# Kernel optimization log

Hardware: AMD Instinct MI355X
Metric: run time of the kernel (lower is better)

Reference implementation:

```python
import jax, jax.numpy as jnp
import numpy as np

B, N, EPG, FDIM, H = 128, 512, 4096, 128, 128
RATIO = 0.5
E = B * EPG
K1 = int(np.ceil(RATIO * N))      # 256
K2 = int(np.ceil(RATIO * K1))     # 128
K3 = int(np.ceil(RATIO * K2))     # 64


def setup_inputs():
    key = jax.random.key(0)
    ks = jax.random.split(key, 12)
    x = jax.random.normal(ks[0], (B * N, FDIM), jnp.float32)
    src = jax.random.randint(ks[1], (B, EPG), 0, N)
    dst = jax.random.randint(ks[2], (B, EPG), 0, N)
    off = (jnp.arange(B) * N)[:, None]
    edge_index = jnp.stack([(src + off).reshape(-1), (dst + off).reshape(-1)], 0).astype(jnp.int32)
    batch = (jnp.arange(B * N) // N).astype(jnp.int32)
    w = lambda k, s: jax.random.normal(k, s, jnp.float32) * 0.05
    return dict(
        x=x, edge_index=edge_index, batch=batch,
        W1=w(ks[3], (FDIM, H)), b1=jnp.zeros((H,), jnp.float32),
        Ws1=w(ks[4], (H, 1)), bs1=jnp.zeros((1,), jnp.float32),
        W2=w(ks[5], (H, H)), b2=jnp.zeros((H,), jnp.float32),
        Ws2=w(ks[6], (H, 1)), bs2=jnp.zeros((1,), jnp.float32),
        W3=w(ks[7], (H, H)), b3=jnp.zeros((H,), jnp.float32),
        Ws3=w(ks[8], (H, 1)), bs3=jnp.zeros((1,), jnp.float32))


def gcn(x, src, dst, emask, W, b):
    # PyG GCNConv: add self-loops, symmetric deg^-1/2 normalization.
    n = x.shape[0]
    h = x @ W
    deg = jnp.zeros((n,), x.dtype).at[dst].add(emask) + 1.0  # +1 for self-loop
    dinv = jax.lax.rsqrt(deg)
    norm = dinv[src] * dinv[dst] * emask                      # masked edges -> 0
    agg = jnp.zeros_like(h).at[dst].add(norm[:, None] * h[src])
    return agg + (dinv * dinv)[:, None] * h + b               # self-loop term + bias


def sag_pool(x, src, dst, emask, Ws, bs, n_per_graph, k):
    n_tot = x.shape[0]
    score = gcn(x, src, dst, emask, Ws, bs)[:, 0]
    sc = score.reshape(B, n_per_graph)
    topv, topi = jax.lax.top_k(sc, k)                         # [B,k] per-graph topk
    xg = x.reshape(B, n_per_graph, -1)
    xnew = jnp.take_along_axis(xg, topi[:, :, None], axis=1) * jnp.tanh(topv)[:, :, None]
    xnew = xnew.reshape(B * k, -1)
    perm = (topi + (jnp.arange(B) * n_per_graph)[:, None]).reshape(-1)
    newidx = jnp.full((n_tot,), -1, jnp.int32).at[perm].set(jnp.arange(B * k, dtype=jnp.int32))
    ns, nd = newidx[src], newidx[dst]
    valid = (ns >= 0) & (nd >= 0)
    emask_new = emask * valid.astype(x.dtype)                 # filter_adj via masking
    ns = jnp.where(valid, ns, 0)
    nd = jnp.where(valid, nd, 0)
    return xnew, ns, nd, emask_new


def readout(x, k):
    xg = x.reshape(B, k, -1)
    return jnp.concatenate([xg.max(axis=1), xg.mean(axis=1)], axis=1)  # [gmp, gap]


def reference(x, edge_index, batch, W1, b1, Ws1, bs1, W2, b2, Ws2, bs2, W3, b3, Ws3, bs3):
    src, dst = edge_index[0], edge_index[1]
    emask = jnp.ones((src.shape[0],), x.dtype)
    h = jax.nn.relu(gcn(x, src, dst, emask, W1, b1))
    h, src, dst, emask = sag_pool(h, src, dst, emask, Ws1, bs1, N, K1)
    x1 = readout(h, K1)
    h = jax.nn.relu(gcn(h, src, dst, emask, W2, b2))
    h, src, dst, emask = sag_pool(h, src, dst, emask, Ws2, bs2, K1, K2)
    x2 = readout(h, K2)
    h = jax.nn.relu(gcn(h, src, dst, emask, W3, b3))
    h, src, dst, emask = sag_pool(h, src, dst, emask, Ws3, bs3, K2, K3)
    x3 = readout(h, K3)
    return x1 + x2 + x3
```

## Files before the change

kernel.cpp:

```cpp
#include <hip/hip_runtime.h>
#include <math.h>

#define BGRAPH 128
#define ETOT   (128*4096)
#define EPG    4096
#define K1 256
#define K2 128
#define K3 64

__global__ __launch_bounds__(256) void gemm_tile3(const float* __restrict__ X,
                                                  const float* __restrict__ W,
                                                  float* __restrict__ Y){
  __shared__ float sA[128][33];
  __shared__ float sB[32][192];
  int t = threadIdx.x;
  int row0 = blockIdx.x * 128;
  int tx = t & 15;
  int ty = t >> 4;
  float acc[8][8];
  #pragma unroll
  for (int i = 0; i < 8; ++i)
    #pragma unroll
    for (int j = 0; j < 8; ++j) acc[i][j] = 0.f;

  for (int k0 = 0; k0 < 128; k0 += 32){
    #pragma unroll
    for (int i = 0; i < 4; ++i){
      int f = t + i*256;
      int row = f >> 3, c4 = f & 7;
      float4 v = *(const float4*)(X + (size_t)(row0 + row)*128 + k0 + c4*4);
      sA[row][c4*4+0] = v.x;
      sA[row][c4*4+1] = v.y;
      sA[row][c4*4+2] = v.z;
      sA[row][c4*4+3] = v.w;
    }
    #pragma unroll
    for (int i = 0; i < 4; ++i){
      int f = t + i*256;
      int kr = f >> 5, c4 = f & 31;
      int gg = c4 >> 1, hh = c4 & 1;
      float4 v = *(const float4*)(W + (size_t)(k0 + kr)*128 + c4*4);
      *(float4*)&sB[kr][gg*12 + hh*4] = v;
    }
    __syncthreads();
    #pragma unroll
    for (int kk = 0; kk < 32; ++kk){
      float4 b0 = *(const float4*)&sB[kk][tx*12];
      float4 b1 = *(const float4*)&sB[kk][tx*12 + 4];
      float aa[8];
      #pragma unroll
      for (int i = 0; i < 8; ++i) aa[i] = sA[ty*8 + i][kk];
      float bb[8] = {b0.x,b0.y,b0.z,b0.w,b1.x,b1.y,b1.z,b1.w};
      #pragma unroll
      for (int i = 0; i < 8; ++i)
        #pragma unroll
        for (int j = 0; j < 8; ++j)
          acc[i][j] = fmaf(aa[i], bb[j], acc[i][j]);
    }
    __syncthreads();
  }
  #pragma unroll
  for (int i = 0; i < 8; ++i){
    float* yr = Y + (size_t)(row0 + ty*8 + i)*128 + tx*8;
    *(float4*)yr       = *(float4*)&acc[i][0];
    *(float4*)(yr + 4) = *(float4*)&acc[i][4];
  }
}

__global__ __launch_bounds__(256) void fused_l1(const float* __restrict__ X,
    const float* __restrict__ W, float* __restrict__ Y,
    const int* __restrict__ src, const int* __restrict__ dst,
    int* __restrict__ off, int* __restrict__ cnt, float* __restrict__ dinv,
    int* __restrict__ csr, int* __restrict__ dsto, float* __restrict__ coef,
    int* __restrict__ ecnt){
  extern __shared__ float smem[];
  int t = threadIdx.x;
  if (blockIdx.x < 512){
    float* sA = smem;
    float* sB = smem + 128*33;
    int row0 = blockIdx.x * 128;
    int tx = t & 15;
    int ty = t >> 4;
    float acc[8][8];
    #pragma unroll
    for (int i = 0; i < 8; ++i)
      #pragma unroll
      for (int j = 0; j < 8; ++j) acc[i][j] = 0.f;

    for (int k0 = 0; k0 < 128; k0 += 32){
      #pragma unroll
      for (int i = 0; i < 4; ++i){
        int f = t + i*256;
        int row = f >> 3, c4 = f & 7;
        float4 v = *(const float4*)(X + (size_t)(row0 + row)*128 + k0 + c4*4);
        sA[row*33 + c4*4+0] = v.x;
        sA[row*33 + c4*4+1] = v.y;
        sA[row*33 + c4*4+2] = v.z;
        sA[row*33 + c4*4+3] = v.w;
      }
      #pragma unroll
      for (int i = 0; i < 4; ++i){
        int f = t + i*256;
        int kr = f >> 5, c4 = f & 31;
        int gg = c4 >> 1, hh = c4 & 1;
        float4 v = *(const float4*)(W + (size_t)(k0 + kr)*128 + c4*4);
        *(float4*)&sB[kr*192 + gg*12 + hh*4] = v;
      }
      __syncthreads();
      #pragma unroll
      for (int kk = 0; kk < 32; ++kk){
        float4 b0 = *(const float4*)&sB[kk*192 + tx*12];
        float4 b1 = *(const float4*)&sB[kk*192 + tx*12 + 4];
        float aa[8];
        #pragma unroll
        for (int i = 0; i < 8; ++i) aa[i] = sA[(ty*8 + i)*33 + kk];
        float bb[8] = {b0.x,b0.y,b0.z,b0.w,b1.x,b1.y,b1.z,b1.w};
        #pragma unroll
        for (int i = 0; i < 8; ++i)
          #pragma unroll
          for (int j = 0; j < 8; ++j)
            acc[i][j] = fmaf(aa[i], bb[j], acc[i][j]);
      }
      __syncthreads();
    }
    #pragma unroll
    for (int i = 0; i < 8; ++i){
      float* yr = Y + (size_t)(row0 + ty*8 + i)*128 + tx*8;
      *(float4*)yr       = *(float4*)&acc[i][0];
      *(float4*)(yr + 4) = *(float4*)&acc[i][4];
    }
  } else {
    int g = blockIdx.x - 512;
    int*   sc  = (int*)smem;
    int*   sp  = sc + 512;
    int*   cur = sp + 256;
    float* sdv = (float*)(cur + 512);
    int*   ss  = (int*)(sdv + 512);
    int*   sd  = ss + 4096;
    sc[t] = 0; sc[t + 256] = 0;
    __syncthreads();
    const int* sg = src + g*EPG;
    const int* dg = dst + g*EPG;
    for (int e = t; e < EPG; e += 256){
      int s = sg[e], d = dg[e];
      ss[e] = s; sd[e] = d;
      atomicAdd(&sc[d & 511], 1);
    }
    __syncthreads();
    int a = sc[2*t], b = sc[2*t+1];
    int pair = a + b;
    sp[t] = pair;
    __syncthreads();
    for (int d = 1; d < 256; d <<= 1){
      int u = (t >= d) ? sp[t-d] : 0;
      __syncthreads();
      sp[t] += u;
      __syncthreads();
    }
    int pre0 = sp[t] - pair;
    int pre1 = pre0 + a;
    float dv0 = rsqrtf((float)a + 1.f);
    float dv1 = rsqrtf((float)b + 1.f);
    sdv[2*t]   = dv0;  sdv[2*t+1] = dv1;
    dinv[g*512 + 2*t]   = dv0;  dinv[g*512 + 2*t+1] = dv1;
    cnt[g*512 + 2*t]    = a;    cnt[g*512 + 2*t+1]  = b;
    off[g*512 + 2*t]    = g*EPG + pre0;
    off[g*512 + 2*t+1]  = g*EPG + pre1;
    sc[2*t] = pre0; sc[2*t+1] = pre1;
    cur[2*t] = 0;   cur[2*t+1] = 0;
    if (t == 0) ecnt[g] = EPG;
    __syncthreads();
    int* cg = csr + g*EPG;
    int* dg2 = dsto + g*EPG;
    float* cf = coef + g*EPG;
    for (int e = t; e < EPG; e += 256){
      int s = ss[e], dl = sd[e] & 511;
      int slot = sc[dl] + atomicAdd(&cur[dl], 1);
      cg[slot]  = s;
      dg2[slot] = g*512 + dl;
      cf[slot]  = sdv[s & 511] * sdv[dl];
    }
  }
}

__global__ void gather_agg(const float* __restrict__ hx, const int* __restrict__ csr,
                           const float* __restrict__ coef,
                           const int* __restrict__ off, const int* __restrict__ cnt,
                           const float* __restrict__ dinv, const float* __restrict__ bias,
                           const float* __restrict__ Ws, float* __restrict__ out,
                           float* __restrict__ hs, int npg, int n){
  int bpg = npg >> 3;
  int x = blockIdx.x >> 3, r = blockIdx.x & 7;
  int pos = x % bpg, grp = x / bpg;
  int g = grp*8 + r;
  int t = threadIdx.x;
  int node = g*npg + pos*8 + (t >> 5);
  int fl = t & 31;
  float dd = dinv[node];
  int o = off[node], deg = cnt[node];
  const float4* rows = (const float4*)hx;
  float4 a0 = {0,0,0,0}, a1 = {0,0,0,0}, a2 = {0,0,0,0}, a3 = {0,0,0,0};
  int e = o, end = o + deg;
  for (; e + 7 < end; e += 8){
    int sx[8]; float cx[8]; float4 vv[8];
    #pragma unroll
    for (int q = 0; q < 8; ++q){ sx[q] = csr[e+q]; cx[q] = coef[e+q]; }
    #pragma unroll
    for (int q = 0; q < 8; ++q) vv[q] = rows[(size_t)sx[q]*32 + fl];
    #pragma unroll
    for (int q = 0; q < 8; ++q){
      float4& aq = (q&3)==0 ? a0 : ((q&3)==1 ? a1 : ((q&3)==2 ? a2 : a3));
      aq.x = fmaf(cx[q], vv[q].x, aq.x);
      aq.y = fmaf(cx[q], vv[q].y, aq.y);
      aq.z = fmaf(cx[q], vv[q].z, aq.z);
      aq.w = fmaf(cx[q], vv[q].w, aq.w);
    }
  }
  for (; e + 3 < end; e += 4){
    int sx[4]; float cx[4]; float4 vv[4];
    #pragma unroll
    for (int q = 0; q < 4; ++q){ sx[q] = csr[e+q]; cx[q] = coef[e+q]; }
    #pragma unroll
    for (int q = 0; q < 4; ++q) vv[q] = rows[(size_t)sx[q]*32 + fl];
    #pragma unroll
    for (int q = 0; q < 4; ++q){
      float4& aq = (q==0) ? a0 : ((q==1) ? a1 : ((q==2) ? a2 : a3));
      aq.x = fmaf(cx[q], vv[q].x, aq.x);
      aq.y = fmaf(cx[q], vv[q].y, aq.y);
      aq.z = fmaf(cx[q], vv[q].z, aq.z);
      aq.w = fmaf(cx[q], vv[q].w, aq.w);
    }
  }
  for (; e < end; ++e){
    int s0 = csr[e];
    float c0 = coef[e];
    float4 v0 = rows[(size_t)s0*32 + fl];
    a0.x=fmaf(c0,v0.x,a0.x); a0.y=fmaf(c0,v0.y,a0.y); a0.z=fmaf(c0,v0.z,a0.z); a0.w=fmaf(c0,v0.w,a0.w);
  }
  float4 own = rows[(size_t)node*32 + fl];
  float4 bv  = ((const float4*)bias)[fl];
  float d2 = dd*dd;
  float4 rr;
  rr.x = fmaxf(fmaf(d2, own.x, (a0.x+a1.x)+(a2.x+a3.x) + bv.x), 0.f);
  rr.y = fmaxf(fmaf(d2, own.y, (a0.y+a1.y)+(a2.y+a3.y) + bv.y), 0.f);
  rr.z = fmaxf(fmaf(d2, own.z, (a0.z+a1.z)+(a2.z+a3.z) + bv.z), 0.f);
  rr.w = fmaxf(fmaf(d2, own.w, (a0.w+a1.w)+(a2.w+a3.w) + bv.w), 0.f);
  ((float4*)(out + (size_t)node*128))[fl] = rr;
  float4 w = ((const float4*)Ws)[fl];
  float p = rr.x*w.x + rr.y*w.y + rr.z*w.z + rr.w*w.w;
  p += __shfl_xor(p, 16);
  p += __shfl_xor(p, 8);
  p += __shfl_xor(p, 4);
  p += __shfl_xor(p, 2);
  p += __shfl_xor(p, 1);
  if (fl == 0) hs[node] = p;
}

template<int NP, int K, int HASNEXT, int FIRST>
__global__ __launch_bounds__(1024) void mega(
    const float* __restrict__ hs, const int* __restrict__ csr_in,
    const int* __restrict__ dst_in, const float* __restrict__ coef_in,
    const int* __restrict__ off_in, const int* __restrict__ cnt_in,
    const float* __restrict__ dinv_in, const float* __restrict__ bs,
    const float* __restrict__ Hm, float* __restrict__ xnew, float* __restrict__ out,
    const int* __restrict__ ecnt_in,
    int* __restrict__ off_o, int* __restrict__ cnt_o, float* __restrict__ dinv_o,
    int* __restrict__ csr_o, int* __restrict__ dst_o, float* __restrict__ coef_o,
    int* __restrict__ ecnt_o)
{
  constexpr int R   = 1024 / NP;
  constexpr int LNP = (NP == 512) ? 9 : ((NP == 256) ? 8 : 7);
  __shared__ int   ss[EPG];
  __shared__ int   sd[EPG];
  __shared__ float scf[EPG];
  __shared__ float shs[NP];
  __shared__ float spart[1024];
  __shared__ float sv[NP];
  __shared__ int   si[NP];
  __shared__ int   lnew[NP];
  __shared__ int   lperm[K];
  __shared__ float ltanh[K];
  __shared__ float smx[1024], ssm[1024];
  __shared__ int   sc[K], sp2[K], cur[K];
  __shared__ float sdvn[K];
  int g = blockIdx.x, t = threadIdx.x;
  int E_in = ecnt_in[g];

  if (t < NP){ shs[t] = hs[g*NP + t]; lnew[t] = -1; }
  for (int e = t; e < E_in; e += 1024){
    ss[e]  = csr_in[g*EPG + e];
    sd[e]  = dst_in[g*EPG + e];
    scf[e] = coef_in[g*EPG + e];
  }
  __syncthreads();

  int n = t & (NP-1);
  int p = t >> LNP;
  {
    int lo = off_in[g*NP + n] - g*EPG, deg = cnt_in[g*NP + n];
    float a = 0.f;
    for (int e = lo + p; e < lo + deg; e += R)
      a = fmaf(scf[e], shs[ss[e] & (NP-1)], a);
    spart[t] = a;
  }
  __syncthreads();
  float v = -INFINITY; int idx = n;
  if (p == 0){
    float a = spart[n];
    #pragma unroll
    for (int q = 1; q < R; ++q) a += spart[n + q*NP];
    float dd = dinv_in[g*NP + n];
    v = a + fmaf(dd*dd, shs[n], bs[0]);
  }
  #pragma unroll
  for (int ksz = 2; ksz <= NP; ksz <<= 1){
    #pragma unroll
    for (int j = ksz >> 1; j > 0; j >>= 1){
      float v2 = 0.f; int i2 = 0;
      if (j >= 64){
        __syncthreads();
        if (t < NP){ sv[t] = v; si[t] = idx; }
        __syncthreads();
        if (t < NP){ v2 = sv[t^j]; i2 = si[t^j]; }
      } else if (t < NP){
        v2 = __shfl_xor(v, j);
        i2 = __shfl_xor(idx, j);
      }
      if (t < NP){
        bool dir = ((t & ksz) == 0);
        bool pf = (v2 > v) || (v2 == v && i2 < idx);
        bool lower = (t & j) == 0;
        if (pf == (lower ? dir : !dir)){ v = v2; idx = i2; }
      }
    }
  }
  if (t < K){
    lperm[t] = idx;
    lnew[idx] = t;
    ltanh[t] = tanhf(v);
  }
  __syncthreads();

  {
    int f = t & 127, q = t >> 7;
    float mx = -INFINITY, sm = 0.f;
    for (int j = q; j < K; j += 8){
      float val = Hm[(size_t)(g*NP + lperm[j])*128 + f] * ltanh[j];
      xnew[(size_t)(g*K + j)*128 + f] = val;
      mx = fmaxf(mx, val); sm += val;
    }
    smx[t] = mx; ssm[t] = sm;
  }
  __syncthreads();
  if (t < 128){
    float mx = smx[t], sm = ssm[t];
    #pragma unroll
    for (int q = 1; q < 8; ++q){ mx = fmaxf(mx, smx[q*128+t]); sm += ssm[q*128+t]; }
    if (FIRST){
      out[g*256 + t]       = mx;
      out[g*256 + 128 + t] = sm / (float)K;
    } else {
      out[g*256 + t]       += mx;
      out[g*256 + 128 + t] += sm / (float)K;
    }
  }
  if (!HASNEXT) return;
  __syncthreads();

  if (t < K) sc[t] = 0;
  __syncthreads();
  for (int e = t; e < E_in; e += 1024){
    int rs = lnew[ss[e] & (NP-1)], rd = lnew[sd[e] & (NP-1)];
    bool ok = (rs | rd) >= 0;
    ss[e] = rs;
    sd[e] = ok ? rd : -1;
    if (ok) atomicAdd(&sc[rd], 1);
  }
  __syncthreads();
  int cv = 0; float dvn = 0.f;
  if (t < K){
    cv = sc[t];
    dvn = rsqrtf((float)cv + 1.f);
    sdvn[t] = dvn;
    dinv_o[g*K + t] = dvn;
    cnt_o[g*K + t] = cv;
    sp2[t] = cv;
  }
  __syncthreads();
  for (int d = 1; d < K; d <<= 1){
    int u = 0;
    if (t >= d && t < K) u = sp2[t-d];
    __syncthreads();
    if (t < K) sp2[t] += u;
    __syncthreads();
  }
  if (t < K){
    int pre = sp2[t] - cv;
    off_o[g*K + t] = g*EPG + pre;
    sc[t] = pre;
    cur[t] = 0;
    if (t == K-1) ecnt_o[g] = pre + cv;
  }
  __syncthreads();
  for (int e = t; e < E_in; e += 1024){
    int ndl = sd[e];
    if (ndl < 0) continue;
    int nsl = ss[e];
    int slot = sc[ndl] + atomicAdd(&cur[ndl], 1);
    csr_o[g*EPG + slot]  = g*K + nsl;
    dst_o[g*EPG + slot]  = g*K + ndl;
    coef_o[g*EPG + slot] = sdvn[nsl] * sdvn[ndl];
  }
}

extern "C" void kernel_launch(void* const* d_in, const int* in_sizes, int n_in,
                              void* d_out, int out_size, void* d_ws, size_t ws_size,
                              hipStream_t stream){
  const float* x0 = (const float*)d_in[0];
  const int*   ei = (const int*)d_in[1];
  const float* Wl[3]  = {(const float*)d_in[3], (const float*)d_in[7],  (const float*)d_in[11]};
  const float* bl[3]  = {(const float*)d_in[4], (const float*)d_in[8],  (const float*)d_in[12]};
  const float* Wsl[3] = {(const float*)d_in[5], (const float*)d_in[9],  (const float*)d_in[13]};
  const float* bsl[3] = {(const float*)d_in[6], (const float*)d_in[10], (const float*)d_in[14]};

  float* A     = (float*)d_ws;
  float* C     = A + (size_t)65536*128;
  float* D     = C + (size_t)65536*128;
  float* dinvA = D + (size_t)32768*128;
  float* dinvB = dinvA + 65536;
  float* hs    = dinvB + 65536;
  int* cntA    = (int*)(hs + 65536);
  int* cntB    = cntA + 65536;
  int* offA    = cntB + 65536;
  int* offB    = offA + 65536;
  int* csrA    = offB + 65536;
  int* csrB    = csrA + ETOT;
  int* dstA    = csrB + ETOT;
  int* dstB    = dstA + ETOT;
  float* coefA = (float*)(dstB + ETOT);
  float* coefB = coefA + ETOT;
  int* ecntA   = (int*)(coefB + ETOT);
  int* ecntB   = ecntA + 128;

  float* out = (float*)d_out;

  size_t shbytes = (size_t)(128*33 + 32*192) * sizeof(float);
  fused_l1<<<640, 256, shbytes, stream>>>(x0, Wl[0], A,
      ei, ei + ETOT, offA, cntA, dinvA, csrA, dstA, coefA, ecntA);
  gather_agg<<<65536/8, 256, 0, stream>>>(A, csrA, coefA, offA, cntA, dinvA, bl[0], Wsl[0], C, hs, 512, 65536);
  mega<512, K1, 1, 1><<<BGRAPH, 1024, 0, stream>>>(hs, csrA, dstA, coefA, offA, cntA, dinvA, bsl[0],
      C, D, out, ecntA, offB, cntB, dinvB, csrB, dstB, coefB, ecntB);
  gemm_tile3<<<32768/128, 256, 0, stream>>>(D, Wl[1], A);
  gather_agg<<<32768/8, 256, 0, stream>>>(A, csrB, coefB, offB, cntB, dinvB, bl[1], Wsl[1], C, hs, 256, 32768);
  mega<256, K2, 1, 0><<<BGRAPH, 1024, 0, stream>>>(hs, csrB, dstB, coefB, offB, cntB, dinvB, bsl[1],
      C, D, out, ecntB, offA, cntA, dinvA, csrA, dstA, coefA, ecntA);
  gemm_tile3<<<16384/128, 256, 0, stream>>>(D, Wl[2], A);
  gather_agg<<<16384/8, 256, 0, stream>>>(A, csrA, coefA, offA, cntA, dinvA, bl[2], Wsl[2], C, hs, 128, 16384);
  mega<128, K3, 0, 0><<<BGRAPH, 1024, 0, stream>>>(hs, csrA, dstA, coefA, offA, cntA, dinvA, bsl[2],
      C, D, out, ecntA, offB, cntB, dinvB, csrB, dstB, coefB, ecntB);
}
```

Before: 183.0 us.

## Shrink GEMM k-tile, drop CSR dst array, read raw edges in first pool

The GEMM k-tile drops from 32 to 16, which halves the shared-memory footprint and should allow more resident blocks. The layer-1 CSR build no longer writes a sorted dst array and no longer stages edges in shared memory; it reads src/dst straight from global memory. The first mega kernel now loads the raw edge lists for filtering and reads CSR coef/index directly from global memory during score aggregation, skipping the shared staging of coefficients. Together these cut memory traffic and shared usage, at the cost of more uncached global loads in the aggregation loop and more k-loop syncs.

```diff
diff --git a/kernel.cpp b/kernel.cpp
--- a/kernel.cpp
+++ b/kernel.cpp
@@ -8,11 +8,11 @@
 #define K2 128
 #define K3 64
 
-__global__ __launch_bounds__(256) void gemm_tile3(const float* __restrict__ X,
-                                                  const float* __restrict__ W,
-                                                  float* __restrict__ Y){
-  __shared__ float sA[128][33];
-  __shared__ float sB[32][192];
+__global__ __launch_bounds__(256) void gemm_bk16(const float* __restrict__ X,
+                                                 const float* __restrict__ W,
+                                                 float* __restrict__ Y){
+  __shared__ float sA[128][17];
+  __shared__ float sB[16][192];
   int t = threadIdx.x;
   int row0 = blockIdx.x * 128;
   int tx = t & 15;
@@ -23,11 +23,11 @@
     #pragma unroll
     for (int j = 0; j < 8; ++j) acc[i][j] = 0.f;
 
-  for (int k0 = 0; k0 < 128; k0 += 32){
-    #pragma unroll
-    for (int i = 0; i < 4; ++i){
+  for (int k0 = 0; k0 < 128; k0 += 16){
+    #pragma unroll
+    for (int i = 0; i < 2; ++i){
       int f = t + i*256;
-      int row = f >> 3, c4 = f & 7;
+      int row = f >> 2, c4 = f & 3;
       float4 v = *(const float4*)(X + (size_t)(row0 + row)*128 + k0 + c4*4);
       sA[row][c4*4+0] = v.x;
       sA[row][c4*4+1] = v.y;
@@ -35,16 +35,15 @@
       sA[row][c4*4+3] = v.w;
     }
     #pragma unroll
-    for (int i = 0; i < 4; ++i){
+    for (int i = 0; i < 2; ++i){
       int f = t + i*256;
       int kr = f >> 5, c4 = f & 31;
-      int gg = c4 >> 1, hh = c4 & 1;
       float4 v = *(const float4*)(W + (size_t)(k0 + kr)*128 + c4*4);
-      *(float4*)&sB[kr][gg*12 + hh*4] = v;
-    }
-    __syncthreads();
-    #pragma unroll
-    for (int kk = 0; kk < 32; ++kk){
+      *(float4*)&sB[kr][(c4>>1)*12 + (c4&1)*4] = v;
+    }
+    __syncthreads();
+    #pragma unroll
+    for (int kk = 0; kk < 16; ++kk){
       float4 b0 = *(const float4*)&sB[kk][tx*12];
       float4 b1 = *(const float4*)&sB[kk][tx*12 + 4];
       float aa[8];
@@ -71,13 +70,12 @@
     const float* __restrict__ W, float* __restrict__ Y,
     const int* __restrict__ src, const int* __restrict__ dst,
     int* __restrict__ off, int* __restrict__ cnt, float* __restrict__ dinv,
-    int* __restrict__ csr, int* __restrict__ dsto, float* __restrict__ coef,
-    int* __restrict__ ecnt){
+    int* __restrict__ csr, float* __restrict__ coef, int* __restrict__ ecnt){
   extern __shared__ float smem[];
   int t = threadIdx.x;
   if (blockIdx.x < 512){
     float* sA = smem;
-    float* sB = smem + 128*33;
+    float* sB = smem + 128*17;
     int row0 = blockIdx.x * 128;
     int tx = t & 15;
     int ty = t >> 4;
@@ -87,33 +85,32 @@
       #pragma unroll
       for (int j = 0; j < 8; ++j) acc[i][j] = 0.f;
 
-    for (int k0 = 0; k0 < 128; k0 += 32){
-      #pragma unroll
-      for (int i = 0; i < 4; ++i){
+    for (int k0 = 0; k0 < 128; k0 += 16){
+      #pragma unroll
+      for (int i = 0; i < 2; ++i){
         int f = t + i*256;
-        int row = f >> 3, c4 = f & 7;
+        int row = f >> 2, c4 = f & 3;
         float4 v = *(const float4*)(X + (size_t)(row0 + row)*128 + k0 + c4*4);
-        sA[row*33 + c4*4+0] = v.x;
-        sA[row*33 + c4*4+1] = v.y;
-        sA[row*33 + c4*4+2] = v.z;
-        sA[row*33 + c4*4+3] = v.w;
+        sA[row*17 + c4*4+0] = v.x;
+        sA[row*17 + c4*4+1] = v.y;
+        sA[row*17 + c4*4+2] = v.z;
+        sA[row*17 + c4*4+3] = v.w;
       }
       #pragma unroll
-      for (int i = 0; i < 4; ++i){
+      for (int i = 0; i < 2; ++i){
         int f = t + i*256;
         int kr = f >> 5, c4 = f & 31;
-        int gg = c4 >> 1, hh = c4 & 1;
         float4 v = *(const float4*)(W + (size_t)(k0 + kr)*128 + c4*4);
-        *(float4*)&sB[kr*192 + gg*12 + hh*4] = v;
+        *(float4*)&sB[kr*192 + (c4>>1)*12 + (c4&1)*4] = v;
       }
       __syncthreads();
       #pragma unroll
-      for (int kk = 0; kk < 32; ++kk){
+      for (int kk = 0; kk < 16; ++kk){
         float4 b0 = *(const float4*)&sB[kk*192 + tx*12];
         float4 b1 = *(const float4*)&sB[kk*192 + tx*12 + 4];
         float aa[8];
         #pragma unroll
-        for (int i = 0; i < 8; ++i) aa[i] = sA[(ty*8 + i)*33 + kk];
+        for (int i = 0; i < 8; ++i) aa[i] = sA[(ty*8 + i)*17 + kk];
         float bb[8] = {b0.x,b0.y,b0.z,b0.w,b1.x,b1.y,b1.z,b1.w};
         #pragma unroll
         for (int i = 0; i < 8; ++i)
@@ -135,17 +132,12 @@
     int*   sp  = sc + 512;
     int*   cur = sp + 256;
     float* sdv = (float*)(cur + 512);
-    int*   ss  = (int*)(sdv + 512);
-    int*   sd  = ss + 4096;
     sc[t] = 0; sc[t + 256] = 0;
     __syncthreads();
     const int* sg = src + g*EPG;
     const int* dg = dst + g*EPG;
-    for (int e = t; e < EPG; e += 256){
-      int s = sg[e], d = dg[e];
-      ss[e] = s; sd[e] = d;
-      atomicAdd(&sc[d & 511], 1);
-    }
+    for (int e = t; e < EPG; e += 256)
+      atomicAdd(&sc[dg[e] & 511], 1);
     __syncthreads();
     int a = sc[2*t], b = sc[2*t+1];
     int pair = a + b;
@@ -171,13 +163,11 @@
     if (t == 0) ecnt[g] = EPG;
     __syncthreads();
     int* cg = csr + g*EPG;
-    int* dg2 = dsto + g*EPG;
     float* cf = coef + g*EPG;
     for (int e = t; e < EPG; e += 256){
-      int s = ss[e], dl = sd[e] & 511;
+      int s = sg[e], dl = dg[e] & 511;
       int slot = sc[dl] + atomicAdd(&cur[dl], 1);
       cg[slot]  = s;
-      dg2[slot] = g*512 + dl;
       cf[slot]  = sdv[s & 511] * sdv[dl];
     }
   }
@@ -256,13 +246,14 @@
   if (fl == 0) hs[node] = p;
 }
 
-template<int NP, int K, int HASNEXT, int FIRST>
+template<int NP, int K, int HASNEXT, int FIRST, int RAW>
 __global__ __launch_bounds__(1024) void mega(
     const float* __restrict__ hs, const int* __restrict__ csr_in,
-    const int* __restrict__ dst_in, const float* __restrict__ coef_in,
-    const int* __restrict__ off_in, const int* __restrict__ cnt_in,
-    const float* __restrict__ dinv_in, const float* __restrict__ bs,
-    const float* __restrict__ Hm, float* __restrict__ xnew, float* __restrict__ out,
+    const float* __restrict__ coef_in, const int* __restrict__ off_in,
+    const int* __restrict__ cnt_in, const float* __restrict__ dinv_in,
+    const float* __restrict__ bs, const float* __restrict__ Hm,
+    float* __restrict__ xnew, float* __restrict__ out,
+    const int* __restrict__ pes, const int* __restrict__ ped,
     const int* __restrict__ ecnt_in,
     int* __restrict__ off_o, int* __restrict__ cnt_o, float* __restrict__ dinv_o,
     int* __restrict__ csr_o, int* __restrict__ dst_o, float* __restrict__ coef_o,
@@ -272,7 +263,7 @@
   constexpr int LNP = (NP == 512) ? 9 : ((NP == 256) ? 8 : 7);
   __shared__ int   ss[EPG];
   __shared__ int   sd[EPG];
-  __shared__ float scf[EPG];
+  __shared__ float scf[RAW ? 1 : EPG];
   __shared__ float shs[NP];
   __shared__ float spart[1024];
   __shared__ float sv[NP];
@@ -288,19 +279,25 @@
 
   if (t < NP){ shs[t] = hs[g*NP + t]; lnew[t] = -1; }
   for (int e = t; e < E_in; e += 1024){
-    ss[e]  = csr_in[g*EPG + e];
-    sd[e]  = dst_in[g*EPG + e];
-    scf[e] = coef_in[g*EPG + e];
+    ss[e] = pes[g*EPG + e];
+    sd[e] = ped[g*EPG + e];
+    if (!RAW) scf[e] = coef_in[g*EPG + e];
   }
   __syncthreads();
 
   int n = t & (NP-1);
   int p = t >> LNP;
   {
-    int lo = off_in[g*NP + n] - g*EPG, deg = cnt_in[g*NP + n];
     float a = 0.f;
-    for (int e = lo + p; e < lo + deg; e += R)
-      a = fmaf(scf[e], shs[ss[e] & (NP-1)], a);
+    if (RAW){
+      int lo = off_in[g*NP + n], deg = cnt_in[g*NP + n];
+      for (int e = lo + p; e < lo + deg; e += R)
+        a = fmaf(coef_in[e], shs[csr_in[e] & (NP-1)], a);
+    } else {
+      int lo = off_in[g*NP + n] - g*EPG, deg = cnt_in[g*NP + n];
+      for (int e = lo + p; e < lo + deg; e += R)
+        a = fmaf(scf[e], shs[ss[e] & (NP-1)], a);
+    }
     spart[t] = a;
   }
   __syncthreads();
@@ -444,18 +441,21 @@
 
   float* out = (float*)d_out;
 
-  size_t shbytes = (size_t)(128*33 + 32*192) * sizeof(float);
+  size_t shbytes = (size_t)(128*17 + 16*192) * sizeof(float);
   fused_l1<<<640, 256, shbytes, stream>>>(x0, Wl[0], A,
-      ei, ei + ETOT, offA, cntA, dinvA, csrA, dstA, coefA, ecntA);
+      ei, ei + ETOT, offA, cntA, dinvA, csrA, coefA, ecntA);
   gather_agg<<<65536/8, 256, 0, stream>>>(A, csrA, coefA, offA, cntA, dinvA, bl[0], Wsl[0], C, hs, 512, 65536);
-  mega<512, K1, 1, 1><<<BGRAPH, 1024, 0, stream>>>(hs, csrA, dstA, coefA, offA, cntA, dinvA, bsl[0],
-      C, D, out, ecntA, offB, cntB, dinvB, csrB, dstB, coefB, ecntB);
-  gemm_tile3<<<32768/128, 256, 0, stream>>>(D, Wl[1], A);
+  mega<512, K1, 1, 1, 1><<<BGRAPH, 1024, 0, stream>>>(hs, csrA, coefA, offA, cntA, dinvA, bsl[0],
+      C, D, out, ei, ei + ETOT, ecntA,
+      offB, cntB, dinvB, csrB, dstB, coefB, ecntB);
+  gemm_bk16<<<32768/128, 256, 0, stream>>>(D, Wl[1], A);
   gather_agg<<<32768/8, 256, 0, stream>>>(A, csrB, coefB, offB, cntB, dinvB, bl[1], Wsl[1], C, hs, 256, 32768);
-  mega<256, K2, 1, 0><<<BGRAPH, 1024, 0, stream>>>(hs, csrB, dstB, coefB, offB, cntB, dinvB, bsl[1],
-      C, D, out, ecntB, offA, cntA, dinvA, csrA, dstA, coefA, ecntA);
-  gemm_tile3<<<16384/128, 256, 0, stream>>>(D, Wl[2], A);
+  mega<256, K2, 1, 0, 0><<<BGRAPH, 1024, 0, stream>>>(hs, csrB, coefB, offB, cntB, dinvB, bsl[1],
+      C, D, out, csrB, dstB, ecntB,
+      offA, cntA, dinvA, csrA, dstA, coefA, ecntA);
+  gemm_bk16<<<16384/128, 256, 0, stream>>>(D, Wl[2], A);
   gather_agg<<<16384/8, 256, 0, stream>>>(A, csrA, coefA, offA, cntA, dinvA, bl[2], Wsl[2], C, hs, 128, 16384);
-  mega<128, K3, 0, 0><<<BGRAPH, 1024, 0, stream>>>(hs, csrA, dstA, coefA, offA, cntA, dinvA, bsl[2],
-      C, D, out, ecntA, offB, cntB, dinvB, csrB, dstB, coefB, ecntB);
+  mega<128, K3, 0, 0, 0><<<BGRAPH, 1024, 0, stream>>>(hs, csrA, coefA, offA, cntA, dinvA, bsl[2],
+      C, D, out, csrA, dstA, ecntA,
+      offB, cntB, dinvB, csrB, dstB, coefB, ecntB);
 }
```

Result: no change. 181.2 us (-1.0%).
